# Performance work log

Measured on AMD Instinct MI355X. Metric: run time of the kernel, lower is better.

## Reference

```python
import jax, jax.numpy as jnp
import numpy as np

HEAD_SIZE = 128
N_EMBED = 2048
B, T = 4, 4096


def setup_inputs() -> dict:
    key = jax.random.key(0)
    kx, kq, kk, kv = jax.random.split(key, 4)
    s = 1.0 / np.sqrt(N_EMBED)
    return {
        "x": jax.random.normal(kx, (B, T, N_EMBED), dtype=jnp.float32),
        "Wq": jax.random.normal(kq, (N_EMBED, HEAD_SIZE), dtype=jnp.float32) * s,
        "Wk": jax.random.normal(kk, (N_EMBED, HEAD_SIZE), dtype=jnp.float32) * s,
        "Wv": jax.random.normal(kv, (N_EMBED, HEAD_SIZE), dtype=jnp.float32) * s,
    }


def reference(x, Wq, Wk, Wv):
    # x: [B, T, C]; projections (no bias)
    q = jnp.einsum('btc,cd->btd', x, Wq)  # [B, T, D]
    k = jnp.einsum('btc,cd->btd', x, Wk)
    v = jnp.einsum('btc,cd->btd', x, Wv)
    scale = q.shape[-1] ** -0.5
    scores = jnp.einsum('btd,bsd->bts', q, k) * scale  # [B, T, T]
    T_ = x.shape[1]
    causal = jnp.tril(jnp.ones((T_, T_), dtype=bool))
    scores = jnp.where(causal, scores, -jnp.inf)
    weight = jax.nn.softmax(scores, axis=-1)
    # dropout is identity in eval mode
    out = jnp.einsum('bts,bsd->btd', weight, v)  # [B, T, D]
    return out
```

## Files before the change

### kernel.cpp

```cpp
#include <hip/hip_runtime.h>
#include <hip/hip_bf16.h>
#include <stdint.h>

typedef unsigned short ushort_t;
typedef short v8s __attribute__((ext_vector_type(8)));
typedef float f32x4 __attribute__((ext_vector_type(4)));
typedef float f32x16 __attribute__((ext_vector_type(16)));

#define MFMA16(a, b, c) __builtin_amdgcn_mfma_f32_16x16x32_bf16(a, b, c, 0, 0, 0)
#define MFMA32(a, b, c) __builtin_amdgcn_mfma_f32_32x32x16_bf16(a, b, c, 0, 0, 0)

typedef __attribute__((address_space(1))) void gvoid;
typedef __attribute__((address_space(3))) void svoid;

__device__ __forceinline__ void gld16(const void* g, void* s) {
    __builtin_amdgcn_global_load_lds((gvoid*)g, (svoid*)s, 16, 0, 0);
}

__device__ __forceinline__ ushort_t f2bf(float f) {
    union { __hip_bfloat16 b; ushort_t u; } c;
    c.b = __float2bfloat16(f);
    return c.u;
}

__device__ __forceinline__ unsigned f2bf2(float a, float b) {
    union { __hip_bfloat162 b2; unsigned u; } c;
    c.b2 = __float22bfloat162_rn(make_float2(a, b));
    return c.u;
}

__global__ void transpose_w(const float* __restrict__ Wq, const float* __restrict__ Wk,
                            const float* __restrict__ Wv, ushort_t* __restrict__ WT) {
    __shared__ float tile[64][132];
    int bid = blockIdx.x;
    int w = bid >> 5;
    int k0 = (bid & 31) << 6;
    const float* W = (w == 0) ? Wq : ((w == 1) ? Wk : Wv);
    int tid = threadIdx.x;
    #pragma unroll
    for (int i = 0; i < 8; i++) {
        int row = i * 8 + (tid >> 5);
        int col = (tid & 31) * 4;
        float4 v = *(const float4*)(W + (size_t)(k0 + row) * 128 + col);
        tile[row][col] = v.x; tile[row][col + 1] = v.y;
        tile[row][col + 2] = v.z; tile[row][col + 3] = v.w;
    }
    __syncthreads();
    int n = tid >> 1, kh = (tid & 1) * 32;
    ushort_t* dst = WT + ((size_t)(w * 128 + n)) * 2048 + k0 + kh;
    #pragma unroll
    for (int j = 0; j < 32; j += 4) {
        union { ushort_t u[4]; uint2 v2; } pk;
        #pragma unroll
        for (int e = 0; e < 4; e++) pk.u[e] = f2bf(tile[kh + j + e][n]);
        *(uint2*)(dst + j) = pk.v2;
    }
}

#define PJ_XLOAD(S, IT)                                                       \
    {                                                                         \
        _Pragma("unroll")                                                     \
        for (int i = 0; i < 4; i++)                                           \
            S[i] = *(const f32x4*)(xsrc[i] + (size_t)(IT) * 256);             \
    }

#define PJ_CVT_WRITE(RS, PAR)                                                 \
    {                                                                         \
        _Pragma("unroll")                                                     \
        for (int i = 0; i < 4; i++) {                                         \
            uint2 p;                                                          \
            p.x = f2bf2(RS[i][0], RS[i][1]);                                  \
            p.y = f2bf2(RS[i][2], RS[i][3]);                                  \
            *(uint2*)((char*)abuf + (PAR) * 16384 + awb[i]) = p;              \
        }                                                                     \
    }

#define PJ_STEP(PAR, IT, RLOAD, RCVT, DOX, DOB)                               \
    {                                                                         \
        if (DOB) {                                                            \
            _Pragma("unroll")                                                 \
            for (int i = 0; i < 3; i++)                                       \
                gld16(bsrc[i] + (size_t)((IT) + 1) * 128,                     \
                      (char*)bbuf + ((PAR) ^ 1) * 24576 + (wid * 3 + i) * 1024); \
        }                                                                     \
        __builtin_amdgcn_sched_barrier(0);                                    \
        if (DOX) PJ_XLOAD(RLOAD, (IT) + 2);                                   \
        __builtin_amdgcn_sched_barrier(0);                                    \
        const char* ab = (const char*)abuf + (PAR) * 16384;                   \
        const char* bb = (const char*)bbuf + (PAR) * 24576;                   \
        _Pragma("unroll")                                                     \
        for (int kk = 0; kk < 2; kk++) {                                      \
            v8s af[4], bf[3];                                                 \
            _Pragma("unroll")                                                 \
            for (int m = 0; m < 4; m++) {                                     \
                int row = wr * 64 + m * 16 + lr;                              \
                af[m] = *(const v8s*)(ab + row * 128 +                        \
                         ((kk * 64 + lg * 16) ^ ((row & 7) << 4)));           \
            }                                                                 \
            _Pragma("unroll")                                                 \
            for (int n = 0; n < 3; n++) {                                     \
                int row = wc * 48 + n * 16 + lr;                              \
                bf[n] = *(const v8s*)(bb + row * 128 +                        \
                         ((kk * 64 + lg * 16) ^ ((row & 7) << 4)));           \
            }                                                                 \
            __builtin_amdgcn_s_setprio(1);                                    \
            _Pragma("unroll")                                                 \
            for (int m = 0; m < 4; m++)                                       \
                _Pragma("unroll")                                             \
                for (int n = 0; n < 3; n++)                                   \
                    acc[m][n] = MFMA16(af[m], bf[n], acc[m][n]);              \
            __builtin_amdgcn_s_setprio(0);                                    \
        }                                                                     \
        if (DOB) {                                                            \
            PJ_CVT_WRITE(RCVT, (PAR) ^ 1);                                    \
            if (DOX) { asm volatile("s_waitcnt vmcnt(4)" ::: "memory"); }     \
            else     { asm volatile("s_waitcnt vmcnt(0)" ::: "memory"); }     \
            asm volatile("s_waitcnt lgkmcnt(0)" ::: "memory");                \
            __builtin_amdgcn_s_barrier();                                     \
        }                                                                     \
    }

__launch_bounds__(512, 1)
__global__ void proj_kernel(const float* __restrict__ x, const ushort_t* __restrict__ WT,
                            ushort_t* __restrict__ q, ushort_t* __restrict__ kb,
                            ushort_t* __restrict__ vb) {
    __shared__ ushort_t abuf[2][8192];
    __shared__ ushort_t bbuf[2][12288];

    int bid = blockIdx.x;
    int xcd = bid & 7, t2 = bid >> 3;
    int nh = t2 & 1, mtl = t2 >> 1;
    int mtile = xcd * 16 + mtl;
    size_t m0 = (size_t)mtile * 128;
    int c0 = nh * 192;
    int tid = threadIdx.x, lane = tid & 63, wid = tid >> 6;
    int lg = lane >> 4, lr = lane & 15;
    int wr = wid >> 2, wc = wid & 3;

    f32x4 acc[4][3];
    #pragma unroll
    for (int m = 0; m < 4; m++)
        #pragma unroll
        for (int n = 0; n < 3; n++) acc[m][n] = (f32x4){0.f, 0.f, 0.f, 0.f};

    const char* xsrc[4];
    int awb[4];
    #pragma unroll
    for (int i = 0; i < 4; i++) {
        int row = 16 * wid + 4 * i + (lane >> 4);
        xsrc[i] = (const char*)x + (m0 + row) * 8192 + (lane & 15) * 16;
        awb[i] = row * 128 + (((lane & 15) * 8) ^ ((row & 7) << 4));
    }

    const char* bsrc[3];
    #pragma unroll
    for (int i = 0; i < 3; i++) {
        int row = 8 * (3 * wid + i) + (lane >> 3);
        int col = ((lane & 7) * 16) ^ ((row & 7) << 4);
        bsrc[i] = (const char*)WT + (size_t)(c0 + row) * 4096 + col;
    }

    f32x4 xs0[4], xs1[4];
    #pragma unroll
    for (int i = 0; i < 3; i++)
        gld16(bsrc[i], (char*)bbuf + (wid * 3 + i) * 1024);
    PJ_XLOAD(xs0, 0);
    PJ_XLOAD(xs1, 1);
    PJ_CVT_WRITE(xs0, 0);
    asm volatile("s_waitcnt vmcnt(0)" ::: "memory");
    asm volatile("s_waitcnt lgkmcnt(0)" ::: "memory");
    __builtin_amdgcn_s_barrier();

    for (int it = 0; it < 30; it += 2) {
        PJ_STEP(0, it,     xs0, xs1, 1, 1);
        PJ_STEP(1, it + 1, xs1, xs0, 1, 1);
    }
    PJ_STEP(0, 30, xs0, xs1, 0, 1);
    PJ_STEP(1, 31, xs1, xs0, 0, 0);

    #pragma unroll
    for (int m = 0; m < 4; m++) {
        #pragma unroll
        for (int e = 0; e < 4; e++) {
            size_t row = m0 + (size_t)(wr * 64 + m * 16 + 4 * lg + e);
            int t = (int)(row & 4095);
            size_t base = (row >> 12) * 524288;
            #pragma unroll
            for (int n = 0; n < 3; n++) {
                int col = c0 + wc * 48 + n * 16 + lr;
                int w = col >> 7, d = col & 127;
                ushort_t val = f2bf(acc[m][n][e]);
                if (w == 0)
                    q[base + (size_t)(t >> 5) * 4096 + (d >> 4) * 512 + ((d >> 3) & 1) * 256 + (t & 31) * 8 + (d & 7)] = val;
                else if (w == 1)
                    kb[base + (size_t)(t >> 5) * 4096 + (d >> 4) * 512 + ((d >> 3) & 1) * 256 + (t & 31) * 8 + (d & 7)] = val;
                else
                    vb[base + (size_t)(t >> 4) * 2048 + (d >> 5) * 512 + ((t >> 3) & 1) * 256 + (d & 31) * 8 + (t & 7)] = val;
            }
        }
    }
}

__device__ __forceinline__ f32x16 zero16() {
    f32x16 z;
    #pragma unroll
    for (int i = 0; i < 16; i++) z[i] = 0.f;
    return z;
}

#define ATT_PVC(SV, BASE, VC, CNEXT)                                          \
    {                                                                         \
        unsigned a0 = f2bf2(SV[(BASE) + 0], SV[(BASE) + 1]);                  \
        unsigned a1 = f2bf2(SV[(BASE) + 2], SV[(BASE) + 3]);                  \
        unsigned b0 = f2bf2(SV[(BASE) + 4], SV[(BASE) + 5]);                  \
        unsigned b1 = f2bf2(SV[(BASE) + 6], SV[(BASE) + 7]);                  \
        unsigned snd0 = hi ? a0 : b0, snd1 = hi ? a1 : b1;                    \
        unsigned rcv0 = (unsigned)__shfl_xor((int)snd0, 32);                  \
        unsigned rcv1 = (unsigned)__shfl_xor((int)snd1, 32);                  \
        union { unsigned u[4]; v8s v; } pf;                                   \
        pf.u[0] = hi ? rcv0 : a0;                                             \
        pf.u[1] = hi ? rcv1 : a1;                                             \
        pf.u[2] = hi ? b0 : rcv0;                                             \
        pf.u[3] = hi ? b1 : rcv1;                                             \
        __builtin_amdgcn_s_setprio(1);                                        \
        _Pragma("unroll")                                                     \
        for (int dt = 0; dt < 4; dt++)                                        \
            accO[dt] = MFMA32(VC[dt], pf.v, accO[dt]);                        \
        __builtin_amdgcn_s_setprio(0);                                        \
        if ((CNEXT) >= 0) {                                                   \
            _Pragma("unroll")                                                 \
            for (int dt = 0; dt < 4; dt++)                                    \
                VC[dt] = *(const v8s*)(vg + (CNEXT) * 2048 + dt * 512);       \
        }                                                                     \
    }

__launch_bounds__(256, 2)
__global__ void attn_kernel(const ushort_t* __restrict__ q, const ushort_t* __restrict__ kb,
                            const ushort_t* __restrict__ vb, float* __restrict__ out) {
    __shared__ float obuf[4][4][16][64];
    __shared__ float stat[2][4][64];

    int bid = blockIdx.x;
    int xcd = bid & 7, rk = bid >> 3;
    int b = xcd >> 1;
    int g = rk * 2 + (xcd & 1);
    int qt = (g & 1) ? (g >> 1) : (127 - (g >> 1));
    int qt0 = qt * 32;
    int tid = threadIdx.x, lane = tid & 63, wid = tid >> 6;
    int hi = lane >> 5, lo = lane & 31;
    size_t bb = (size_t)b * 524288;
    int nt = (qt >> 1) + 1;
    const float cexp = 0.08838834764831845f * 1.4426950408889634f;

    v8s qf[8];
    {
        const ushort_t* qg = q + bb + (size_t)qt * 4096 + (size_t)lane * 8;
        #pragma unroll
        for (int ks = 0; ks < 8; ks++) qf[ks] = *(const v8s*)(qg + ks * 512);
    }

    f32x16 accO[4];
    #pragma unroll
    for (int dt = 0; dt < 4; dt++) accO[dt] = zero16();
    float mrun = -1e30f, lrun = 0.f;

    for (int t = wid; t < nt; t += 4) {
        const ushort_t* kg = kb + bb + (size_t)t * 8192 + (size_t)lane * 8;
        const ushort_t* vg = vb + bb + (size_t)t * 8192 + (size_t)lane * 8;

        f32x16 s0 = zero16(), s1 = zero16();
        __builtin_amdgcn_s_setprio(1);
        #pragma unroll
        for (int ks = 0; ks < 8; ks++) {
            v8s kf = *(const v8s*)(kg + ks * 512);
            s0 = MFMA32(kf, qf[ks], s0);
        }
        #pragma unroll
        for (int ks = 0; ks < 8; ks++) {
            v8s kf = *(const v8s*)(kg + 4096 + ks * 512);
            s1 = MFMA32(kf, qf[ks], s1);
        }
        __builtin_amdgcn_s_setprio(0);

        v8s vA[4], vB[4];
        #pragma unroll
        for (int dt = 0; dt < 4; dt++) vA[dt] = *(const v8s*)(vg + dt * 512);
        #pragma unroll
        for (int dt = 0; dt < 4; dt++) vB[dt] = *(const v8s*)(vg + 2048 + dt * 512);

        if (t == nt - 1) {
            int qrow = qt0 + lo;
            #pragma unroll
            for (int r = 0; r < 16; r++) {
                int kvb = t * 64 + (r & 3) + 8 * (r >> 2) + 4 * hi;
                if (kvb > qrow) s0[r] = -1e30f;
                if (kvb + 32 > qrow) s1[r] = -1e30f;
            }
        }

        float mx = s0[0];
        #pragma unroll
        for (int r = 1; r < 16; r++) mx = fmaxf(mx, s0[r]);
        #pragma unroll
        for (int r = 0; r < 16; r++) mx = fmaxf(mx, s1[r]);
        mx = fmaxf(mx, __shfl_xor(mx, 32));

        if (__any(mx > mrun + 62.7f)) {
            float mnew = fmaxf(mrun, mx);
            float fr = exp2f((mrun - mnew) * cexp);
            lrun *= fr;
            #pragma unroll
            for (int dt = 0; dt < 4; dt++)
                #pragma unroll
                for (int r = 0; r < 16; r++) accO[dt][r] *= fr;
            mrun = mnew;
        }
        float mc = mrun * cexp;
        float rs = 0.f;
        #pragma unroll
        for (int r = 0; r < 16; r++) { s0[r] = exp2f(fmaf(s0[r], cexp, -mc)); rs += s0[r]; }
        #pragma unroll
        for (int r = 0; r < 16; r++) { s1[r] = exp2f(fmaf(s1[r], cexp, -mc)); rs += s1[r]; }
        rs += __shfl_xor(rs, 32);
        lrun += rs;

        ATT_PVC(s0, 0, vA, 2);
        ATT_PVC(s0, 8, vB, 3);
        ATT_PVC(s1, 0, vA, -1);
        ATT_PVC(s1, 8, vB, -1);
    }

    #pragma unroll
    for (int dt = 0; dt < 4; dt++)
        #pragma unroll
        for (int r = 0; r < 16; r++)
            obuf[wid][dt][r][lane] = accO[dt][r];
    stat[0][wid][lane] = mrun;
    stat[1][wid][lane] = lrun;
    __syncthreads();

    float m0 = stat[0][0][lane], m1 = stat[0][1][lane];
    float m2 = stat[0][2][lane], m3 = stat[0][3][lane];
    float m = fmaxf(fmaxf(m0, m1), fmaxf(m2, m3));
    float f0 = exp2f((m0 - m) * cexp), f1 = exp2f((m1 - m) * cexp);
    float f2 = exp2f((m2 - m) * cexp), f3 = exp2f((m3 - m) * cexp);
    float lsum = f0 * stat[1][0][lane] + f1 * stat[1][1][lane]
               + f2 * stat[1][2][lane] + f3 * stat[1][3][lane];
    float linv = 1.0f / lsum;

    float o[16];
    #pragma unroll
    for (int r = 0; r < 16; r++)
        o[r] = (f0 * obuf[0][wid][r][lane] + f1 * obuf[1][wid][r][lane]
              + f2 * obuf[2][wid][r][lane] + f3 * obuf[3][wid][r][lane]) * linv;

    float* orow = out + ((size_t)b * 4096 + qt0 + lo) * 128 + wid * 32 + 4 * hi;
    #pragma unroll
    for (int a = 0; a < 4; a++) {
        float4 vv;
        vv.x = o[4 * a + 0]; vv.y = o[4 * a + 1];
        vv.z = o[4 * a + 2]; vv.w = o[4 * a + 3];
        *(float4*)(orow + 8 * a) = vv;
    }
}

extern "C" void kernel_launch(void* const* d_in, const int* in_sizes, int n_in,
                              void* d_out, int out_size, void* d_ws, size_t ws_size,
                              hipStream_t stream) {
    const float* x  = (const float*)d_in[0];
    const float* Wq = (const float*)d_in[1];
    const float* Wk = (const float*)d_in[2];
    const float* Wv = (const float*)d_in[3];
    float* out = (float*)d_out;
    char* ws = (char*)d_ws;

    ushort_t* q  = (ushort_t*)(ws);
    ushort_t* kb = (ushort_t*)(ws + (4u << 20));
    ushort_t* vb = (ushort_t*)(ws + (8u << 20));
    ushort_t* WT = (ushort_t*)(ws + (12u << 20));

    transpose_w<<<dim3(96), dim3(256), 0, stream>>>(Wq, Wk, Wv, WT);
    proj_kernel<<<dim3(256), dim3(512), 0, stream>>>(x, WT, q, kb, vb);
    attn_kernel<<<dim3(512), dim3(256), 0, stream>>>(q, kb, vb, out);
}
```

Before: 101.8 us.

## Split projection k-step into two barrier-separated phases interleaving loads with MFMA

The projection GEMM main loop is restructured into two half-k phases per tile. Each phase issues its LDS fragment reads first, then global/LDS-bound loads or conversion writes, then runs MFMAs between workgroup barriers. The intent is a ping-pong style schedule in which memory issue and matrix math from different waves overlap more regularly. It adds extra s_barrier calls per tile, which may cost synchronization time in a kernel limited to one block per CU.

```diff
diff --git a/kernel.cpp b/kernel.cpp
--- a/kernel.cpp
+++ b/kernel.cpp
@@ -75,8 +75,22 @@
         }                                                                     \
     }
 
-#define PJ_STEP(PAR, IT, RLOAD, RCVT, DOX, DOB)                               \
+#define PJ_PHASE1(PAR, IT, DOB)                                               \
     {                                                                         \
+        const char* ab = (const char*)abuf + (PAR) * 16384;                   \
+        const char* bb = (const char*)bbuf + (PAR) * 24576;                   \
+        v8s af[4], bf[3];                                                     \
+        _Pragma("unroll")                                                     \
+        for (int m = 0; m < 4; m++) {                                         \
+            int row = wr * 64 + m * 16 + lr;                                  \
+            af[m] = *(const v8s*)(ab + row * 128 + ((lg * 16) ^ ((row & 7) << 4))); \
+        }                                                                     \
+        _Pragma("unroll")                                                     \
+        for (int n = 0; n < 3; n++) {                                         \
+            int row = wc * 48 + n * 16 + lr;                                  \
+            bf[n] = *(const v8s*)(bb + row * 128 + ((lg * 16) ^ ((row & 7) << 4))); \
+        }                                                                     \
+        __builtin_amdgcn_sched_barrier(0);                                    \
         if (DOB) {                                                            \
             _Pragma("unroll")                                                 \
             for (int i = 0; i < 3; i++)                                       \
@@ -84,41 +98,59 @@
                       (char*)bbuf + ((PAR) ^ 1) * 24576 + (wid * 3 + i) * 1024); \
         }                                                                     \
         __builtin_amdgcn_sched_barrier(0);                                    \
-        if (DOX) PJ_XLOAD(RLOAD, (IT) + 2);                                   \
-        __builtin_amdgcn_sched_barrier(0);                                    \
+        __builtin_amdgcn_s_barrier();                                         \
+        asm volatile("s_waitcnt lgkmcnt(0)" ::: "memory");                    \
+        __builtin_amdgcn_sched_barrier(0);                                    \
+        __builtin_amdgcn_s_setprio(1);                                        \
+        _Pragma("unroll")                                                     \
+        for (int m = 0; m < 4; m++)                                           \
+            _Pragma("unroll")                                                 \
+            for (int n = 0; n < 3; n++)                                       \
+                acc[m][n] = MFMA16(af[m], bf[n], acc[m][n]);                  \
+        __builtin_amdgcn_s_setprio(0);                                        \
+        __builtin_amdgcn_s_barrier();                                         \
+    }
+
+#define PJ_PHASE2(PAR, IT, RLOAD, RCVT, DOX, DOB)                             \
+    {                                                                         \
         const char* ab = (const char*)abuf + (PAR) * 16384;                   \
         const char* bb = (const char*)bbuf + (PAR) * 24576;                   \
-        _Pragma("unroll")                                                     \
-        for (int kk = 0; kk < 2; kk++) {                                      \
-            v8s af[4], bf[3];                                                 \
-            _Pragma("unroll")                                                 \
-            for (int m = 0; m < 4; m++) {                                     \
-                int row = wr * 64 + m * 16 + lr;                              \
-                af[m] = *(const v8s*)(ab + row * 128 +                        \
-                         ((kk * 64 + lg * 16) ^ ((row & 7) << 4)));           \
-            }                                                                 \
-            _Pragma("unroll")                                                 \
-            for (int n = 0; n < 3; n++) {                                     \
-                int row = wc * 48 + n * 16 + lr;                              \
-                bf[n] = *(const v8s*)(bb + row * 128 +                        \
-                         ((kk * 64 + lg * 16) ^ ((row & 7) << 4)));           \
-            }                                                                 \
-            __builtin_amdgcn_s_setprio(1);                                    \
-            _Pragma("unroll")                                                 \
-            for (int m = 0; m < 4; m++)                                       \
-                _Pragma("unroll")                                             \
-                for (int n = 0; n < 3; n++)                                   \
-                    acc[m][n] = MFMA16(af[m], bf[n], acc[m][n]);              \
-            __builtin_amdgcn_s_setprio(0);                                    \
-        }                                                                     \
+        v8s af[4], bf[3];                                                     \
+        _Pragma("unroll")                                                     \
+        for (int m = 0; m < 4; m++) {                                         \
+            int row = wr * 64 + m * 16 + lr;                                  \
+            af[m] = *(const v8s*)(ab + row * 128 + ((64 + lg * 16) ^ ((row & 7) << 4))); \
+        }                                                                     \
+        _Pragma("unroll")                                                     \
+        for (int n = 0; n < 3; n++) {                                         \
+            int row = wc * 48 + n * 16 + lr;                                  \
+            bf[n] = *(const v8s*)(bb + row * 128 + ((64 + lg * 16) ^ ((row & 7) << 4))); \
+        }                                                                     \
+        __builtin_amdgcn_sched_barrier(0);                                    \
+        if (DOX) PJ_XLOAD(RLOAD, (IT) + 2);                                   \
+        __builtin_amdgcn_sched_barrier(0);                                    \
+        if (DOB) PJ_CVT_WRITE(RCVT, (PAR) ^ 1);                               \
+        __builtin_amdgcn_sched_barrier(0);                                    \
         if (DOB) {                                                            \
-            PJ_CVT_WRITE(RCVT, (PAR) ^ 1);                                    \
             if (DOX) { asm volatile("s_waitcnt vmcnt(4)" ::: "memory"); }     \
             else     { asm volatile("s_waitcnt vmcnt(0)" ::: "memory"); }     \
-            asm volatile("s_waitcnt lgkmcnt(0)" ::: "memory");                \
-            __builtin_amdgcn_s_barrier();                                     \
-        }                                                                     \
-    }
+        }                                                                     \
+        __builtin_amdgcn_s_barrier();                                         \
+        asm volatile("s_waitcnt lgkmcnt(0)" ::: "memory");                    \
+        __builtin_amdgcn_sched_barrier(0);                                    \
+        __builtin_amdgcn_s_setprio(1);                                        \
+        _Pragma("unroll")                                                     \
+        for (int m = 0; m < 4; m++)                                           \
+            _Pragma("unroll")                                                 \
+            for (int n = 0; n < 3; n++)                                       \
+                acc[m][n] = MFMA16(af[m], bf[n], acc[m][n]);                  \
+        __builtin_amdgcn_s_setprio(0);                                        \
+        __builtin_amdgcn_s_barrier();                                         \
+    }
+
+#define PJ_TILE(PAR, IT, RLOAD, RCVT, DOX, DOB)                               \
+    PJ_PHASE1(PAR, IT, DOB)                                                   \
+    PJ_PHASE2(PAR, IT, RLOAD, RCVT, DOX, DOB)
 
 __launch_bounds__(512, 1)
 __global__ void proj_kernel(const float* __restrict__ x, const ushort_t* __restrict__ WT,
@@ -171,12 +203,12 @@
     asm volatile("s_waitcnt lgkmcnt(0)" ::: "memory");
     __builtin_amdgcn_s_barrier();
 
-    for (int it = 0; it < 30; it += 2) {
-        PJ_STEP(0, it,     xs0, xs1, 1, 1);
-        PJ_STEP(1, it + 1, xs1, xs0, 1, 1);
-    }
-    PJ_STEP(0, 30, xs0, xs1, 0, 1);
-    PJ_STEP(1, 31, xs1, xs0, 0, 0);
+    for (int t = 0; t < 30; t += 2) {
+        PJ_TILE(0, t,     xs0, xs1, 1, 1);
+        PJ_TILE(1, t + 1, xs1, xs0, 1, 1);
+    }
+    PJ_TILE(0, 30, xs0, xs1, 0, 1);
+    PJ_TILE(1, 31, xs1, xs0, 0, 0);
 
     #pragma unroll
     for (int m = 0; m < 4; m++) {
```

Measured after the change: 91.83 us. 1.11x faster.
